# Optimization experiments

Hardware: AMD Instinct MI355X
Metric: run time of the kernel (lower is better)

The kernel has to match this reference:

```python
import jax, jax.numpy as jnp
import numpy as np

BN_EPS = 1e-5

def _vq(x, embed):
    # x: (..., dim), embed: (dim, K). Nearest-codeword lookup with straight-through.
    dim = x.shape[-1]
    flat = x.reshape(-1, dim)
    dist = (flat * flat).sum(1, keepdims=True) - 2.0 * (flat @ embed) + (embed * embed).sum(0, keepdims=True)
    ids = jnp.argmin(dist, axis=1)
    q = jnp.take(embed.T, ids, axis=0).reshape(x.shape)
    diff = jnp.mean((jax.lax.stop_gradient(q) - x) ** 2)
    q = x + jax.lax.stop_gradient(q - x)
    return q, diff

def _weight_quantize(W, embed, in_mem, out_mem):
    # W: (out_f, in_f). Group W.T into (out_g, in_g, in_mem*out_mem) blocks,
    # VQ each block, scatter back to (out_f, in_f). Matches torch chunk/stack loops.
    out_f, in_f = W.shape
    in_g, out_g = in_f // in_mem, out_f // out_mem
    g = W.T.reshape(in_g, in_mem, out_g, out_mem).transpose(2, 0, 1, 3).reshape(out_g, in_g, in_mem * out_mem)
    q, diff = _vq(g, embed)
    qW = q.reshape(out_g, in_g, in_mem, out_mem).transpose(0, 3, 1, 2).reshape(out_f, in_f)
    return qW, diff

def _bn(x, gamma, beta):
    # training-mode BatchNorm1d: biased batch variance
    mu = x.mean(axis=0)
    var = ((x - mu) ** 2).mean(axis=0)
    return (x - mu) * jax.lax.rsqrt(var + BN_EPS) * gamma + beta


def setup_inputs() -> dict:
    key = jax.random.key(0)
    ks = jax.random.split(key, 8)
    B, D_IN, H, D_OUT, K = 65536, 784, 512, 10, 512
    s = 0.05
    return {
        "x": jax.random.normal(ks[0], (B, D_IN), jnp.float32),
        "W1": jax.random.normal(ks[1], (H, D_IN), jnp.float32) * s,
        "b1": jnp.zeros((H,), jnp.float32),
        "gamma1": jnp.ones((H,), jnp.float32),
        "beta1": jnp.zeros((H,), jnp.float32),
        "E1": jax.random.normal(ks[2], (28, K), jnp.float32) * s,  # dim = in_mem(7)*out_mem(4)
        "W2": jax.random.normal(ks[3], (H, H), jnp.float32) * s,
        "b2": jnp.zeros((H,), jnp.float32),
        "E2": jax.random.normal(ks[4], (16, K), jnp.float32) * s,  # dim = in_mem(16)*out_mem(1)
        "W3": jax.random.normal(ks[5], (D_OUT, H), jnp.float32) * s,
        "b3": jnp.zeros((D_OUT,), jnp.float32),
    }


def reference(x, W1, b1, gamma1, beta1, E1, W2, b2, E2, W3, b3):
    qW1, diff1 = _weight_quantize(W1, E1, 7, 4)
    h = jax.nn.relu(x @ qW1.T + b1)
    qW2, diff2 = _weight_quantize(W2, E2, 16, 1)
    h = jax.nn.relu(_bn(h, gamma1, beta1) @ qW2.T + b2)
    out = h @ W3.T + b3
    return out, diff1 + diff2
```

## Files before the change

### kernel.cpp

```cpp
#include <hip/hip_runtime.h>
#include <stdint.h>

#define BATCH   65536
#define D_IN    784
#define KP      800
#define HDIM    512
#define D_OUT   10
#define NCODE   512
#define HT_LD   136

typedef _Float16 f16;
typedef _Float16 f16x8 __attribute__((ext_vector_type(8)));
typedef float    f32x4 __attribute__((ext_vector_type(4)));

__device__ __forceinline__ void gld_lds16(const void* g, void* l) {
  __builtin_amdgcn_global_load_lds((const __attribute__((address_space(1))) void*)g,
                                   (__attribute__((address_space(3))) void*)l, 16, 0, 0);
}

#define MEMFENCE asm volatile("" ::: "memory")
#define BARRIER() do { MEMFENCE; __builtin_amdgcn_s_barrier(); MEMFENCE; } while (0)

__global__ void k_vq1(const float* __restrict__ W1, const float* __restrict__ E1,
                      f16* __restrict__ qW1, float* __restrict__ diffacc) {
  #pragma clang fp contract(off)
  __shared__ float E1s[28 * NCODE];
  __shared__ float Ts[NCODE];
  for (int i = threadIdx.x; i < 28 * NCODE; i += 256) E1s[i] = E1[i];
  __syncthreads();
  for (int k = threadIdx.x; k < NCODE; k += 256) {
    float e0 = E1s[k];
    float t = e0 * e0;
    for (int j = 1; j < 28; ++j) {
      float e = E1s[j * NCODE + k];
      float ee = e * e;
      t = t + ee;
    }
    Ts[k] = t;
  }
  __syncthreads();
  const int wid = threadIdx.x >> 6, lane = threadIdx.x & 63;
  const int bid = blockIdx.x * 4 + wid;
  const int og = bid / 112, ig = bid % 112;
  float v[28], vv[28];
  #pragma unroll
  for (int j = 0; j < 28; ++j) {
    int om = j & 3, im = j >> 2;
    v[j] = W1[(og * 4 + om) * D_IN + ig * 7 + im];
    vv[j] = v[j] * v[j];
  }
  float r[8];
  #pragma unroll
  for (int j = 0; j < 8; ++j) r[j] = vv[j];
  #pragma unroll
  for (int j = 0; j < 8; ++j) r[j] = r[j] + vv[8 + j];
  #pragma unroll
  for (int j = 0; j < 8; ++j) r[j] = r[j] + vv[16 + j];
  float s = ((r[0] + r[1]) + (r[2] + r[3])) + ((r[4] + r[5]) + (r[6] + r[7]));
  s = s + vv[24]; s = s + vv[25]; s = s + vv[26]; s = s + vv[27];

  float bestd = 1e30f; int bestk = 0x7fffffff;
  for (int t = 0; t < 8; ++t) {
    int k = t * 64 + lane;
    float dot = 0.f;
    #pragma unroll
    for (int j = 0; j < 28; ++j) dot = __builtin_fmaf(v[j], E1s[j * NCODE + k], dot);
    float d = (s - 2.0f * dot) + Ts[k];
    if (d < bestd || (d == bestd && k < bestk)) { bestd = d; bestk = k; }
  }
  for (int off = 32; off; off >>= 1) {
    float d2 = __shfl_down(bestd, off, 64);
    int   k2 = __shfl_down(bestk, off, 64);
    if (d2 < bestd || (d2 == bestd && k2 < bestk)) { bestd = d2; bestk = k2; }
  }
  int kstar = __shfl(bestk, 0, 64);
  float sq = 0.f;
  if (lane < 28) {
    int om = lane & 3, im = lane >> 2;
    float q = E1s[lane * NCODE + kstar];
    qW1[(size_t)(og * 4 + om) * KP + ig * 7 + im] = (f16)q;
    float dd = q - v[lane]; sq = dd * dd;
  }
  for (int off = 32; off; off >>= 1) sq += __shfl_down(sq, off, 64);
  if (lane == 0) atomicAdd(&diffacc[bid & 127], sq);
}

__global__ void k_vq2(const float* __restrict__ W2, const float* __restrict__ E2,
                      f16* __restrict__ qW2, float* __restrict__ diffacc) {
  #pragma clang fp contract(off)
  __shared__ float E2s[16 * NCODE];
  __shared__ float Ts[NCODE];
  for (int i = threadIdx.x; i < 16 * NCODE; i += 256) E2s[i] = E2[i];
  __syncthreads();
  for (int k = threadIdx.x; k < NCODE; k += 256) {
    float e0 = E2s[k];
    float t = e0 * e0;
    for (int j = 1; j < 16; ++j) {
      float e = E2s[j * NCODE + k];
      float ee = e * e;
      t = t + ee;
    }
    Ts[k] = t;
  }
  __syncthreads();
  const int wid = threadIdx.x >> 6, lane = threadIdx.x & 63;
  const int bid = blockIdx.x * 4 + wid;
  const int og = bid >> 5, ig = bid & 31;
  float v[16], vv[16];
  #pragma unroll
  for (int j = 0; j < 16; ++j) {
    v[j] = W2[og * HDIM + ig * 16 + j];
    vv[j] = v[j] * v[j];
  }
  float r[8];
  #pragma unroll
  for (int j = 0; j < 8; ++j) r[j] = vv[j];
  #pragma unroll
  for (int j = 0; j < 8; ++j) r[j] = r[j] + vv[8 + j];
  float s = ((r[0] + r[1]) + (r[2] + r[3])) + ((r[4] + r[5]) + (r[6] + r[7]));

  float bestd = 1e30f; int bestk = 0x7fffffff;
  for (int t = 0; t < 8; ++t) {
    int k = t * 64 + lane;
    float dot = 0.f;
    #pragma unroll
    for (int j = 0; j < 16; ++j) dot = __builtin_fmaf(v[j], E2s[j * NCODE + k], dot);
    float d = (s - 2.0f * dot) + Ts[k];
    if (d < bestd || (d == bestd && k < bestk)) { bestd = d; bestk = k; }
  }
  for (int off = 32; off; off >>= 1) {
    float d2 = __shfl_down(bestd, off, 64);
    int   k2 = __shfl_down(bestk, off, 64);
    if (d2 < bestd || (d2 == bestd && k2 < bestk)) { bestd = d2; bestk = k2; }
  }
  int kstar = __shfl(bestk, 0, 64);
  float sq = 0.f;
  if (lane < 16) {
    float q = E2s[lane * NCODE + kstar];
    qW2[(size_t)og * HDIM + ig * 16 + lane] = (f16)q;
    float dd = q - v[lane]; sq = dd * dd;
  }
  for (int off = 32; off; off >>= 1) sq += __shfl_down(sq, off, 64);
  if (lane == 0) atomicAdd(&diffacc[bid & 127], sq);
}

__global__ void __launch_bounds__(256, 4)
k_gemm1(const float* __restrict__ X, const f16* __restrict__ Bw,
        const float* __restrict__ bias, f16* __restrict__ C,
        float* __restrict__ statacc) {
  __shared__ __align__(16) char lds_all[HT_LD * 128 * 2];
  __shared__ float cls[128], cls2[128];
  f16* ht = (f16*)lds_all;
  const int tid = threadIdx.x;
  const int logical = ((blockIdx.x & 7) << 8) + (blockIdx.x >> 3);
  const int bn = logical & 3;
  const int bm = logical >> 2;
  const int lane = tid & 63, wid = tid >> 6;
  const int waveM = wid & 1, waveN = wid >> 1;
  const int l15 = lane & 15, quad = lane >> 4;

  if (tid < 128) cls[tid] = 0.f; else cls2[tid - 128] = 0.f;

  const int cA = tid & 3;
  const int r0 = tid >> 2;
  const float* gX0 = X + (size_t)(bm * 128 + r0) * D_IN;
  const float* gX1 = gX0 + (size_t)64 * D_IN;
  const f16*  gB0 = Bw + (size_t)(bn * 128 + r0) * KP + cA * 8;
  const f16*  gB1 = gB0 + (size_t)64 * KP;

  f32x4 acc[4][4];
  #pragma unroll
  for (int i = 0; i < 4; ++i)
    #pragma unroll
    for (int j = 0; j < 4; ++j) acc[i][j] = (f32x4){0.f, 0.f, 0.f, 0.f};

  const int aoff = (waveM * 64 + l15) * 32 + quad * 8;
  const int boff = (waveN * 64 + l15) * 32 + quad * 8;

  float4 ra0, ra1, ra2, ra3;
  auto issueA = [&](int k0) {
    int gc = k0 + cA * 8;
    int gco = gc < D_IN ? gc : 0;
    ra0 = *(const float4*)(gX0 + gco);
    ra1 = *(const float4*)(gX0 + gco + 4);
    ra2 = *(const float4*)(gX1 + gco);
    ra3 = *(const float4*)(gX1 + gco + 4);
  };
  auto writeA = [&](int k0, f16* dstA) {
    bool valid = (k0 + cA * 8) < D_IN;
    float4 a0 = ra0, a1 = ra1, b0 = ra2, b1 = ra3;
    if (!valid) {
      a0 = (float4){0.f,0.f,0.f,0.f}; a1 = a0; b0 = a0; b1 = a0;
    }
    f16x8 o0, o1;
    o0[0]=(f16)a0.x; o0[1]=(f16)a0.y; o0[2]=(f16)a0.z; o0[3]=(f16)a0.w;
    o0[4]=(f16)a1.x; o0[5]=(f16)a1.y; o0[6]=(f16)a1.z; o0[7]=(f16)a1.w;
    o1[0]=(f16)b0.x; o1[1]=(f16)b0.y; o1[2]=(f16)b0.z; o1[3]=(f16)b0.w;
    o1[4]=(f16)b1.x; o1[5]=(f16)b1.y; o1[6]=(f16)b1.z; o1[7]=(f16)b1.w;
    *(f16x8*)(dstA + tid * 8) = o0;
    *(f16x8*)(dstA + tid * 8 + 2048) = o1;
  };
  auto issueB = [&](int k0, f16* dstB) {
    gld_lds16(gB0 + k0, dstB + tid * 8);
    gld_lds16(gB1 + k0, dstB + tid * 8 + 2048);
  };
  auto mma = [&](const f16* A_, const f16* B_) {
    f16x8 af[4], bf[4];
    #pragma unroll
    for (int i = 0; i < 4; ++i) af[i] = *(const f16x8*)(A_ + aoff + i * 512);
    #pragma unroll
    for (int j = 0; j < 4; ++j) bf[j] = *(const f16x8*)(B_ + boff + j * 512);
    #pragma unroll
    for (int i = 0; i < 4; ++i)
      #pragma unroll
      for (int j = 0; j < 4; ++j)
        acc[i][j] = __builtin_amdgcn_mfma_f32_16x16x32_f16(af[i], bf[j], acc[i][j], 0, 0, 0);
  };

  const int NT = KP / 32;
  issueA(0);
  MEMFENCE;
  issueB(0, (f16*)(lds_all + 16384));
  MEMFENCE;
  writeA(0, (f16*)lds_all);
  issueA(32);
  asm volatile("s_waitcnt vmcnt(4) lgkmcnt(0)" ::: "memory");
  BARRIER();

  for (int k = 0; k < NT; ++k) {
    const int cur = k & 1;
    f16* Asc = (f16*)(lds_all + cur * 8192);
    f16* Bsc = (f16*)(lds_all + 16384 + cur * 8192);
    f16* Asn = (f16*)(lds_all + (cur ^ 1) * 8192);
    f16* Bsn = (f16*)(lds_all + 16384 + (cur ^ 1) * 8192);
    if (k + 1 < NT) issueB((k + 1) * 32, Bsn);
    MEMFENCE;
    __builtin_amdgcn_s_setprio(1);
    mma(Asc, Bsc);
    __builtin_amdgcn_s_setprio(0);
    if (k + 1 < NT) {
      writeA((k + 1) * 32, Asn);
      if (k + 2 < NT) {
        issueA((k + 2) * 32);
        asm volatile("s_waitcnt vmcnt(4) lgkmcnt(0)" ::: "memory");
      } else {
        asm volatile("s_waitcnt vmcnt(0) lgkmcnt(0)" ::: "memory");
      }
    }
    BARRIER();
  }
  const int colbase = bn * 128 + waveN * 64 + l15;
  float bcol[4];
  #pragma unroll
  for (int j = 0; j < 4; ++j) bcol[j] = bias[colbase + j * 16];
  float cs[4] = {0.f,0.f,0.f,0.f}, cs2[4] = {0.f,0.f,0.f,0.f};
  #pragma unroll
  for (int i = 0; i < 4; ++i)
    #pragma unroll
    for (int r2 = 0; r2 < 4; ++r2) {
      int rloc = waveM * 64 + quad * 4 + i * 16 + r2;
      #pragma unroll
      for (int j = 0; j < 4; ++j) {
        float v = acc[i][j][r2] + bcol[j];
        v = v > 0.f ? v : 0.f;
        ht[rloc * HT_LD + waveN * 64 + j * 16 + l15] = (f16)v;
        cs[j] += v; cs2[j] += v * v;
      }
    }
  #pragma unroll
  for (int j = 0; j < 4; ++j) {
    cs[j]  += __shfl_xor(cs[j], 16, 64);  cs[j]  += __shfl_xor(cs[j], 32, 64);
    cs2[j] += __shfl_xor(cs2[j], 16, 64); cs2[j] += __shfl_xor(cs2[j], 32, 64);
  }
  if (quad == 0) {
    #pragma unroll
    for (int j = 0; j < 4; ++j) {
      atomicAdd(&cls[waveN * 64 + j * 16 + l15], cs[j]);
      atomicAdd(&cls2[waveN * 64 + j * 16 + l15], cs2[j]);
    }
  }
  __syncthreads();
  if (tid < 128) atomicAdd(&statacc[256 + bn * 128 + tid], cls[tid]);
  else           atomicAdd(&statacc[768 + bn * 128 + (tid - 128)], cls2[tid - 128]);
  {
    const int rloc = tid >> 1, half = tid & 1;
    f16* crow = C + (size_t)(bm * 128 + rloc) * HDIM + bn * 128 + half * 64;
    const f16* srow = ht + rloc * HT_LD + half * 64;
    #pragma unroll
    for (int j = 0; j < 8; ++j)
      *(f16x8*)(crow + j * 8) = *(const f16x8*)(srow + j * 8);
  }
}

__global__ void k_bnprep(const float* __restrict__ acc, const float* __restrict__ gamma,
                         const float* __restrict__ beta, float* __restrict__ ab,
                         const float* __restrict__ W3, f16* __restrict__ W3h,
                         float* __restrict__ diff_out) {
  const int c = threadIdx.x;
  const float inv = 1.f / 65536.f;
  float mu = acc[256 + c] * inv;
  float msq = acc[768 + c] * inv;
  float var = msq - mu * mu;
  float a = gamma[c] / sqrtf(var + 1e-5f);
  ab[c] = a;
  ab[512 + c] = beta[c] - mu * a;
  #pragma unroll
  for (int o = 0; o < 16; ++o)
    W3h[o * HDIM + c] = (o < D_OUT) ? (f16)W3[o * HDIM + c] : (f16)0.f;
  if (c == 0) {
    float s1 = 0.f, s2 = 0.f;
    for (int i = 0; i < 128; ++i) { s1 += acc[i]; s2 += acc[128 + i]; }
    diff_out[0] = s1 * (1.f / 401408.f) + s2 * (1.f / 262144.f);
  }
}

__global__ void k_bnfold(f16* __restrict__ qW2, const float* __restrict__ ab,
                         const float* __restrict__ b2, float* __restrict__ bias2) {
  __shared__ float red[256];
  const int n = blockIdx.x, t = threadIdx.x;
  float partial = 0.f;
  #pragma unroll
  for (int kk = 0; kk < 2; ++kk) {
    int k = t + kk * 256;
    float w = (float)qW2[n * HDIM + k];
    partial += ab[512 + k] * w;
    qW2[n * HDIM + k] = (f16)(ab[k] * w);
  }
  red[t] = partial; __syncthreads();
  for (int s = 128; s > 0; s >>= 1) { if (t < s) red[t] += red[t + s]; __syncthreads(); }
  if (t == 0) bias2[n] = b2[n] + red[0];
}

__global__ void __launch_bounds__(256, 4)
k_gemm2f(const f16* __restrict__ A, const f16* __restrict__ Bw,
         const float* __restrict__ bias2, const f16* __restrict__ W3h,
         const float* __restrict__ b3, float* __restrict__ out) {
  __shared__ __align__(16) char lds_all[HT_LD * 128 * 2];
  f16* ht = (f16*)lds_all;
  const int tid = threadIdx.x;
  const int logical = ((blockIdx.x & 7) << 8) + (blockIdx.x >> 3);
  const int bn = logical & 3;
  const int bm = logical >> 2;
  const int lane = tid & 63, wid = tid >> 6;
  const int waveM = wid & 1, waveN = wid >> 1;
  const int l15 = lane & 15, quad = lane >> 4;

  const f16* gA0 = A  + (size_t)(bm * 128 + (tid >> 2)) * HDIM + (tid & 3) * 8;
  const f16* gA1 = gA0 + (size_t)64 * HDIM;
  const f16* gB0 = Bw + (size_t)(bn * 128 + (tid >> 2)) * HDIM + (tid & 3) * 8;
  const f16* gB1 = gB0 + (size_t)64 * HDIM;

  f32x4 acc[4][4];
  #pragma unroll
  for (int i = 0; i < 4; ++i)
    #pragma unroll
    for (int j = 0; j < 4; ++j) acc[i][j] = (f32x4){0.f, 0.f, 0.f, 0.f};

  const int aoff = (waveM * 64 + l15) * 32 + quad * 8;
  const int boff = (waveN * 64 + l15) * 32 + quad * 8;

  auto issueT = [&](int k0, int b) {
    f16* As_ = (f16*)(lds_all + b * 8192);
    f16* Bs_ = (f16*)(lds_all + 16384 + b * 8192);
    gld_lds16(gA0 + k0, As_ + tid * 8);
    gld_lds16(gA1 + k0, As_ + tid * 8 + 2048);
    gld_lds16(gB0 + k0, Bs_ + tid * 8);
    gld_lds16(gB1 + k0, Bs_ + tid * 8 + 2048);
  };
  auto mma = [&](const f16* A_, const f16* B_) {
    f16x8 af[4], bf[4];
    #pragma unroll
    for (int i = 0; i < 4; ++i) af[i] = *(const f16x8*)(A_ + aoff + i * 512);
    #pragma unroll
    for (int j = 0; j < 4; ++j) bf[j] = *(const f16x8*)(B_ + boff + j * 512);
    #pragma unroll
    for (int i = 0; i < 4; ++i)
      #pragma unroll
      for (int j = 0; j < 4; ++j)
        acc[i][j] = __builtin_amdgcn_mfma_f32_16x16x32_f16(af[i], bf[j], acc[i][j], 0, 0, 0);
  };

  const int NT = HDIM / 32;
  issueT(0, 0);
  asm volatile("s_waitcnt vmcnt(0)" ::: "memory");
  BARRIER();

  for (int k = 0; k < NT; ++k) {
    const int cur = k & 1;
    if (k + 1 < NT) issueT((k + 1) * 32, cur ^ 1);
    MEMFENCE;
    __builtin_amdgcn_s_setprio(1);
    mma((f16*)(lds_all + cur * 8192), (f16*)(lds_all + 16384 + cur * 8192));
    __builtin_amdgcn_s_setprio(0);
    if (k + 1 < NT) asm volatile("s_waitcnt vmcnt(0)" ::: "memory");
    BARRIER();
  }
  const int colbase = bn * 128 + waveN * 64 + l15;
  float bcol[4];
  #pragma unroll
  for (int j = 0; j < 4; ++j) bcol[j] = bias2[colbase + j * 16];
  #pragma unroll
  for (int i = 0; i < 4; ++i)
    #pragma unroll
    for (int r2 = 0; r2 < 4; ++r2) {
      int rloc = waveM * 64 + quad * 4 + i * 16 + r2;
      #pragma unroll
      for (int j = 0; j < 4; ++j) {
        float v = acc[i][j][r2] + bcol[j];
        v = v > 0.f ? v : 0.f;
        ht[rloc * HT_LD + waveN * 64 + j * 16 + l15] = (f16)v;
      }
    }
  __syncthreads();
  f32x4 oacc[2];
  oacc[0] = (f32x4){0.f,0.f,0.f,0.f}; oacc[1] = (f32x4){0.f,0.f,0.f,0.f};
  #pragma unroll
  for (int ks = 0; ks < 4; ++ks) {
    f16x8 bfr = *(const f16x8*)(W3h + l15 * HDIM + bn * 128 + ks * 32 + quad * 8);
    #pragma unroll
    for (int i2 = 0; i2 < 2; ++i2) {
      f16x8 afr = *(const f16x8*)(ht + (wid * 32 + i2 * 16 + l15) * HT_LD + ks * 32 + quad * 8);
      oacc[i2] = __builtin_amdgcn_mfma_f32_16x16x32_f16(afr, bfr, oacc[i2], 0, 0, 0);
    }
  }
  if (l15 < D_OUT) {
    float badd = (bn == 0) ? b3[l15] : 0.f;
    #pragma unroll
    for (int i2 = 0; i2 < 2; ++i2)
      #pragma unroll
      for (int r2 = 0; r2 < 4; ++r2) {
        int row = bm * 128 + wid * 32 + i2 * 16 + quad * 4 + r2;
        atomicAdd(&out[(size_t)row * D_OUT + l15], oacc[i2][r2] + badd);
      }
  }
}

extern "C" void kernel_launch(void* const* d_in, const int* in_sizes, int n_in,
                              void* d_out, int out_size, void* d_ws, size_t ws_size,
                              hipStream_t stream) {
  const float* x     = (const float*)d_in[0];
  const float* W1    = (const float*)d_in[1];
  const float* b1    = (const float*)d_in[2];
  const float* gamma = (const float*)d_in[3];
  const float* beta  = (const float*)d_in[4];
  const float* E1    = (const float*)d_in[5];
  const float* W2    = (const float*)d_in[6];
  const float* b2    = (const float*)d_in[7];
  const float* E2    = (const float*)d_in[8];
  const float* W3    = (const float*)d_in[9];
  const float* b3    = (const float*)d_in[10];
  float* out = (float*)d_out;

  char* ws = (char*)d_ws;
  float* accum = (float*)ws;
  f16* qW1h = (f16*)(ws + 8192);
  f16* qW2h = (f16*)(ws + 827392);
  f16* W3h  = (f16*)(ws + 1351680);
  float* ab = (float*)(ws + 1368064);
  float* bias2 = (float*)(ws + 1372160);
  f16* h    = (f16*)(ws + 1376256);

  hipMemsetAsync(ws, 0, 827392, stream);
  hipMemsetAsync(d_out, 0, (size_t)out_size * 4, stream);
  k_vq1<<<3584, 256, 0, stream>>>(W1, E1, qW1h, accum);
  k_vq2<<<4096, 256, 0, stream>>>(W2, E2, qW2h, accum + 128);
  k_gemm1<<<2048, 256, 0, stream>>>(x, qW1h, b1, h, accum);
  k_bnprep<<<1, 512, 0, stream>>>(accum, gamma, beta, ab, W3, W3h, out + (size_t)BATCH * D_OUT);
  k_bnfold<<<512, 256, 0, stream>>>(qW2h, ab, b2, bias2);
  k_gemm2f<<<2048, 256, 0, stream>>>(h, qW2h, bias2, W3h, b3, out);
}
```

Measured before the change: 545.9 us.

## Make each GEMM block own a full 128x512 row tile with triple-buffered swizzled LDS

Both GEMM kernels are restructured so that one 512-thread block computes all 512 output columns for its 128 rows, instead of four 256-thread blocks each computing 128 columns. In GEMM1 this removes the fourfold re-read and re-conversion of the fp32 X rows. In the fused second GEMM it lets the final 512-to-10 projection be done entirely inside one block, so outputs are stored directly, with no atomics and no memset of the output. The K loop now uses a three-stage LDS ring that prefetches two steps ahead, with an XOR swizzle on the LDS column chunks to reduce bank conflicts. In exchange it uses far more LDS and registers per block, so occupancy drops to roughly one block per CU and the grid has only 512 blocks.

```diff
diff --git a/kernel.cpp b/kernel.cpp
--- a/kernel.cpp
+++ b/kernel.cpp
@@ -7,7 +7,7 @@
 #define HDIM    512
 #define D_OUT   10
 #define NCODE   512
-#define HT_LD   136
+#define HT_LD   520
 
 typedef _Float16 f16;
 typedef _Float16 f16x8 __attribute__((ext_vector_type(8)));
@@ -144,151 +144,154 @@
   if (lane == 0) atomicAdd(&diffacc[bid & 127], sq);
 }
 
-__global__ void __launch_bounds__(256, 4)
+__global__ void __launch_bounds__(512, 2)
 k_gemm1(const float* __restrict__ X, const f16* __restrict__ Bw,
         const float* __restrict__ bias, f16* __restrict__ C,
         float* __restrict__ statacc) {
   __shared__ __align__(16) char lds_all[HT_LD * 128 * 2];
-  __shared__ float cls[128], cls2[128];
+  __shared__ float cls[512], cls2[512];
   f16* ht = (f16*)lds_all;
   const int tid = threadIdx.x;
-  const int logical = ((blockIdx.x & 7) << 8) + (blockIdx.x >> 3);
-  const int bn = logical & 3;
-  const int bm = logical >> 2;
+  const int bm = blockIdx.x;
   const int lane = tid & 63, wid = tid >> 6;
   const int waveM = wid & 1, waveN = wid >> 1;
   const int l15 = lane & 15, quad = lane >> 4;
 
-  if (tid < 128) cls[tid] = 0.f; else cls2[tid - 128] = 0.f;
-
-  const int cA = tid & 3;
-  const int r0 = tid >> 2;
-  const float* gX0 = X + (size_t)(bm * 128 + r0) * D_IN;
-  const float* gX1 = gX0 + (size_t)64 * D_IN;
-  const f16*  gB0 = Bw + (size_t)(bn * 128 + r0) * KP + cA * 8;
-  const f16*  gB1 = gB0 + (size_t)64 * KP;
-
-  f32x4 acc[4][4];
+  cls[tid] = 0.f; cls2[tid] = 0.f;
+
+  const int rA = tid >> 2, cA = tid & 3;
+  const float* gArow = X + (size_t)(bm * 128 + rA) * D_IN;
+  const int wAoff = rA * 32 + ((cA ^ ((rA >> 1) & 3)) * 8);
+  const f16* gBp[4]; int lBoff[4];
+  #pragma unroll
+  for (int i = 0; i < 4; ++i) {
+    int s = tid + i * 512;
+    int rB = s >> 2, cB = s & 3;
+    gBp[i] = Bw + (size_t)rB * KP + ((cB ^ ((rB >> 1) & 3)) * 8);
+    lBoff[i] = s * 8;
+  }
+
+  f32x4 acc[4][8];
   #pragma unroll
   for (int i = 0; i < 4; ++i)
     #pragma unroll
-    for (int j = 0; j < 4; ++j) acc[i][j] = (f32x4){0.f, 0.f, 0.f, 0.f};
-
-  const int aoff = (waveM * 64 + l15) * 32 + quad * 8;
-  const int boff = (waveN * 64 + l15) * 32 + quad * 8;
-
-  float4 ra0, ra1, ra2, ra3;
+    for (int j = 0; j < 8; ++j) acc[i][j] = (f32x4){0.f, 0.f, 0.f, 0.f};
+
+  const int cs_l = (l15 >> 1) & 3;
+  const int aoff = (waveM * 64 + l15) * 32;
+  const int boff = (waveN * 128 + l15) * 32;
+  const int qoff = (quad ^ cs_l) * 8;
+
+  float4 ra0, ra1;
   auto issueA = [&](int k0) {
     int gc = k0 + cA * 8;
     int gco = gc < D_IN ? gc : 0;
-    ra0 = *(const float4*)(gX0 + gco);
-    ra1 = *(const float4*)(gX0 + gco + 4);
-    ra2 = *(const float4*)(gX1 + gco);
-    ra3 = *(const float4*)(gX1 + gco + 4);
-  };
-  auto writeA = [&](int k0, f16* dstA) {
-    bool valid = (k0 + cA * 8) < D_IN;
-    float4 a0 = ra0, a1 = ra1, b0 = ra2, b1 = ra3;
-    if (!valid) {
-      a0 = (float4){0.f,0.f,0.f,0.f}; a1 = a0; b0 = a0; b1 = a0;
-    }
-    f16x8 o0, o1;
-    o0[0]=(f16)a0.x; o0[1]=(f16)a0.y; o0[2]=(f16)a0.z; o0[3]=(f16)a0.w;
-    o0[4]=(f16)a1.x; o0[5]=(f16)a1.y; o0[6]=(f16)a1.z; o0[7]=(f16)a1.w;
-    o1[0]=(f16)b0.x; o1[1]=(f16)b0.y; o1[2]=(f16)b0.z; o1[3]=(f16)b0.w;
-    o1[4]=(f16)b1.x; o1[5]=(f16)b1.y; o1[6]=(f16)b1.z; o1[7]=(f16)b1.w;
-    *(f16x8*)(dstA + tid * 8) = o0;
-    *(f16x8*)(dstA + tid * 8 + 2048) = o1;
-  };
-  auto issueB = [&](int k0, f16* dstB) {
-    gld_lds16(gB0 + k0, dstB + tid * 8);
-    gld_lds16(gB1 + k0, dstB + tid * 8 + 2048);
-  };
-  auto mma = [&](const f16* A_, const f16* B_) {
-    f16x8 af[4], bf[4];
-    #pragma unroll
-    for (int i = 0; i < 4; ++i) af[i] = *(const f16x8*)(A_ + aoff + i * 512);
-    #pragma unroll
-    for (int j = 0; j < 4; ++j) bf[j] = *(const f16x8*)(B_ + boff + j * 512);
+    ra0 = *(const float4*)(gArow + gco);
+    ra1 = *(const float4*)(gArow + gco + 4);
+  };
+  auto writeA = [&](int k0, char* buf) {
+    float4 a0 = ra0, a1 = ra1;
+    if (k0 + cA * 8 >= D_IN) { a0 = (float4){0.f,0.f,0.f,0.f}; a1 = a0; }
+    f16x8 o;
+    o[0]=(f16)a0.x; o[1]=(f16)a0.y; o[2]=(f16)a0.z; o[3]=(f16)a0.w;
+    o[4]=(f16)a1.x; o[5]=(f16)a1.y; o[6]=(f16)a1.z; o[7]=(f16)a1.w;
+    *(f16x8*)((f16*)buf + wAoff) = o;
+  };
+  auto issueB = [&](int k0, char* buf) {
+    f16* Bs_ = (f16*)(buf + 8192);
+    #pragma unroll
+    for (int i = 0; i < 4; ++i) gld_lds16(gBp[i] + k0, Bs_ + lBoff[i]);
+  };
+  auto mma = [&](const char* buf) {
+    const f16* As_ = (const f16*)buf;
+    const f16* Bs_ = (const f16*)(buf + 8192);
+    f16x8 af[4], bf[8];
+    #pragma unroll
+    for (int i = 0; i < 4; ++i) af[i] = *(const f16x8*)(As_ + aoff + i * 512 + qoff);
+    #pragma unroll
+    for (int j = 0; j < 8; ++j) bf[j] = *(const f16x8*)(Bs_ + boff + j * 512 + qoff);
     #pragma unroll
     for (int i = 0; i < 4; ++i)
       #pragma unroll
-      for (int j = 0; j < 4; ++j)
+      for (int j = 0; j < 8; ++j)
         acc[i][j] = __builtin_amdgcn_mfma_f32_16x16x32_f16(af[i], bf[j], acc[i][j], 0, 0, 0);
   };
 
   const int NT = KP / 32;
-  issueA(0);
+
+  issueA(0);  MEMFENCE;
+  issueB(0, lds_all);          MEMFENCE;
+  issueB(32, lds_all + 40960); MEMFENCE;
+  writeA(0, lds_all);
   MEMFENCE;
-  issueB(0, (f16*)(lds_all + 16384));
-  MEMFENCE;
-  writeA(0, (f16*)lds_all);
-  issueA(32);
-  asm volatile("s_waitcnt vmcnt(4) lgkmcnt(0)" ::: "memory");
+  issueA(32); MEMFENCE;
+  asm volatile("s_waitcnt vmcnt(6) lgkmcnt(0)" ::: "memory");
   BARRIER();
 
+  int cur = 0;
   for (int k = 0; k < NT; ++k) {
-    const int cur = k & 1;
-    f16* Asc = (f16*)(lds_all + cur * 8192);
-    f16* Bsc = (f16*)(lds_all + 16384 + cur * 8192);
-    f16* Asn = (f16*)(lds_all + (cur ^ 1) * 8192);
-    f16* Bsn = (f16*)(lds_all + 16384 + (cur ^ 1) * 8192);
-    if (k + 1 < NT) issueB((k + 1) * 32, Bsn);
+    int n1 = cur + 40960; if (n1 == 122880) n1 = 0;
+    int n2 = n1 + 40960;  if (n2 == 122880) n2 = 0;
+    if (k + 2 < NT) { issueB((k + 2) * 32, lds_all + n2); }
     MEMFENCE;
     __builtin_amdgcn_s_setprio(1);
-    mma(Asc, Bsc);
+    mma(lds_all + cur);
     __builtin_amdgcn_s_setprio(0);
     if (k + 1 < NT) {
-      writeA((k + 1) * 32, Asn);
+      MEMFENCE;
+      writeA((k + 1) * 32, lds_all + n1);
+      MEMFENCE;
       if (k + 2 < NT) {
-        issueA((k + 2) * 32);
-        asm volatile("s_waitcnt vmcnt(4) lgkmcnt(0)" ::: "memory");
+        issueA((k + 2) * 32); MEMFENCE;
+        asm volatile("s_waitcnt vmcnt(6) lgkmcnt(0)" ::: "memory");
       } else {
         asm volatile("s_waitcnt vmcnt(0) lgkmcnt(0)" ::: "memory");
       }
     }
     BARRIER();
-  }
-  const int colbase = bn * 128 + waveN * 64 + l15;
-  float bcol[4];
-  #pragma unroll
-  for (int j = 0; j < 4; ++j) bcol[j] = bias[colbase + j * 16];
-  float cs[4] = {0.f,0.f,0.f,0.f}, cs2[4] = {0.f,0.f,0.f,0.f};
+    cur = n1;
+  }
+
+  const int colbase = waveN * 128 + l15;
+  float bcol[8];
+  #pragma unroll
+  for (int j = 0; j < 8; ++j) bcol[j] = bias[colbase + j * 16];
+  float cs[8], cs2[8];
+  #pragma unroll
+  for (int j = 0; j < 8; ++j) { cs[j] = 0.f; cs2[j] = 0.f; }
   #pragma unroll
   for (int i = 0; i < 4; ++i)
     #pragma unroll
     for (int r2 = 0; r2 < 4; ++r2) {
-      int rloc = waveM * 64 + quad * 4 + i * 16 + r2;
+      int rloc = waveM * 64 + i * 16 + quad * 4 + r2;
       #pragma unroll
-      for (int j = 0; j < 4; ++j) {
+      for (int j = 0; j < 8; ++j) {
         float v = acc[i][j][r2] + bcol[j];
         v = v > 0.f ? v : 0.f;
-        ht[rloc * HT_LD + waveN * 64 + j * 16 + l15] = (f16)v;
+        ht[rloc * HT_LD + waveN * 128 + j * 16 + l15] = (f16)v;
         cs[j] += v; cs2[j] += v * v;
       }
     }
   #pragma unroll
-  for (int j = 0; j < 4; ++j) {
+  for (int j = 0; j < 8; ++j) {
     cs[j]  += __shfl_xor(cs[j], 16, 64);  cs[j]  += __shfl_xor(cs[j], 32, 64);
     cs2[j] += __shfl_xor(cs2[j], 16, 64); cs2[j] += __shfl_xor(cs2[j], 32, 64);
   }
   if (quad == 0) {
     #pragma unroll
-    for (int j = 0; j < 4; ++j) {
-      atomicAdd(&cls[waveN * 64 + j * 16 + l15], cs[j]);
-      atomicAdd(&cls2[waveN * 64 + j * 16 + l15], cs2[j]);
-    }
-  }
-  __syncthreads();
-  if (tid < 128) atomicAdd(&statacc[256 + bn * 128 + tid], cls[tid]);
-  else           atomicAdd(&statacc[768 + bn * 128 + (tid - 128)], cls2[tid - 128]);
-  {
-    const int rloc = tid >> 1, half = tid & 1;
-    f16* crow = C + (size_t)(bm * 128 + rloc) * HDIM + bn * 128 + half * 64;
-    const f16* srow = ht + rloc * HT_LD + half * 64;
-    #pragma unroll
-    for (int j = 0; j < 8; ++j)
-      *(f16x8*)(crow + j * 8) = *(const f16x8*)(srow + j * 8);
+    for (int j = 0; j < 8; ++j) {
+      atomicAdd(&cls[waveN * 128 + j * 16 + l15], cs[j]);
+      atomicAdd(&cls2[waveN * 128 + j * 16 + l15], cs2[j]);
+    }
+  }
+  __syncthreads();
+  atomicAdd(&statacc[256 + tid], cls[tid]);
+  atomicAdd(&statacc[768 + tid], cls2[tid]);
+  #pragma unroll
+  for (int rr = 0; rr < 16; ++rr) {
+    int row = wid * 16 + rr;
+    f16x8 vrow = *(const f16x8*)(ht + row * HT_LD + lane * 8);
+    *(f16x8*)(C + (size_t)(bm * 128 + row) * HDIM + lane * 8) = vrow;
   }
 }
 
@@ -331,107 +334,116 @@
   if (t == 0) bias2[n] = b2[n] + red[0];
 }
 
-__global__ void __launch_bounds__(256, 4)
+__global__ void __launch_bounds__(512, 2)
 k_gemm2f(const f16* __restrict__ A, const f16* __restrict__ Bw,
          const float* __restrict__ bias2, const f16* __restrict__ W3h,
          const float* __restrict__ b3, float* __restrict__ out) {
   __shared__ __align__(16) char lds_all[HT_LD * 128 * 2];
   f16* ht = (f16*)lds_all;
   const int tid = threadIdx.x;
-  const int logical = ((blockIdx.x & 7) << 8) + (blockIdx.x >> 3);
-  const int bn = logical & 3;
-  const int bm = logical >> 2;
+  const int bm = blockIdx.x;
   const int lane = tid & 63, wid = tid >> 6;
   const int waveM = wid & 1, waveN = wid >> 1;
   const int l15 = lane & 15, quad = lane >> 4;
 
-  const f16* gA0 = A  + (size_t)(bm * 128 + (tid >> 2)) * HDIM + (tid & 3) * 8;
-  const f16* gA1 = gA0 + (size_t)64 * HDIM;
-  const f16* gB0 = Bw + (size_t)(bn * 128 + (tid >> 2)) * HDIM + (tid & 3) * 8;
-  const f16* gB1 = gB0 + (size_t)64 * HDIM;
-
-  f32x4 acc[4][4];
+  const int rA = tid >> 2, cA = tid & 3;
+  const f16* gAp = A + (size_t)(bm * 128 + rA) * HDIM + ((cA ^ ((rA >> 1) & 3)) * 8);
+  const int lAoff = tid * 8;
+  const f16* gBp[4]; int lBoff[4];
+  #pragma unroll
+  for (int i = 0; i < 4; ++i) {
+    int s = tid + i * 512;
+    int rB = s >> 2, cB = s & 3;
+    gBp[i] = Bw + (size_t)rB * HDIM + ((cB ^ ((rB >> 1) & 3)) * 8);
+    lBoff[i] = s * 8;
+  }
+
+  f32x4 acc[4][8];
   #pragma unroll
   for (int i = 0; i < 4; ++i)
     #pragma unroll
-    for (int j = 0; j < 4; ++j) acc[i][j] = (f32x4){0.f, 0.f, 0.f, 0.f};
-
-  const int aoff = (waveM * 64 + l15) * 32 + quad * 8;
-  const int boff = (waveN * 64 + l15) * 32 + quad * 8;
-
-  auto issueT = [&](int k0, int b) {
-    f16* As_ = (f16*)(lds_all + b * 8192);
-    f16* Bs_ = (f16*)(lds_all + 16384 + b * 8192);
-    gld_lds16(gA0 + k0, As_ + tid * 8);
-    gld_lds16(gA1 + k0, As_ + tid * 8 + 2048);
-    gld_lds16(gB0 + k0, Bs_ + tid * 8);
-    gld_lds16(gB1 + k0, Bs_ + tid * 8 + 2048);
-  };
-  auto mma = [&](const f16* A_, const f16* B_) {
-    f16x8 af[4], bf[4];
-    #pragma unroll
-    for (int i = 0; i < 4; ++i) af[i] = *(const f16x8*)(A_ + aoff + i * 512);
-    #pragma unroll
-    for (int j = 0; j < 4; ++j) bf[j] = *(const f16x8*)(B_ + boff + j * 512);
+    for (int j = 0; j < 8; ++j) acc[i][j] = (f32x4){0.f, 0.f, 0.f, 0.f};
+
+  const int cs_l = (l15 >> 1) & 3;
+  const int aoff = (waveM * 64 + l15) * 32;
+  const int boff = (waveN * 128 + l15) * 32;
+  const int qoff = (quad ^ cs_l) * 8;
+
+  auto issueT = [&](int k0, char* buf) {
+    f16* As_ = (f16*)buf;
+    f16* Bs_ = (f16*)(buf + 8192);
+    gld_lds16(gAp + k0, As_ + lAoff);
+    #pragma unroll
+    for (int i = 0; i < 4; ++i) gld_lds16(gBp[i] + k0, Bs_ + lBoff[i]);
+  };
+  auto mma = [&](const char* buf) {
+    const f16* As_ = (const f16*)buf;
+    const f16* Bs_ = (const f16*)(buf + 8192);
+    f16x8 af[4], bf[8];
+    #pragma unroll
+    for (int i = 0; i < 4; ++i) af[i] = *(const f16x8*)(As_ + aoff + i * 512 + qoff);
+    #pragma unroll
+    for (int j = 0; j < 8; ++j) bf[j] = *(const f16x8*)(Bs_ + boff + j * 512 + qoff);
     #pragma unroll
     for (int i = 0; i < 4; ++i)
       #pragma unroll
-      for (int j = 0; j < 4; ++j)
+      for (int j = 0; j < 8; ++j)
         acc[i][j] = __builtin_amdgcn_mfma_f32_16x16x32_f16(af[i], bf[j], acc[i][j], 0, 0, 0);
   };
 
   const int NT = HDIM / 32;
-  issueT(0, 0);
-  asm volatile("s_waitcnt vmcnt(0)" ::: "memory");
+
+  issueT(0, lds_all);          MEMFENCE;
+  issueT(32, lds_all + 40960); MEMFENCE;
+  asm volatile("s_waitcnt vmcnt(5)" ::: "memory");
   BARRIER();
 
+  int cur = 0;
   for (int k = 0; k < NT; ++k) {
-    const int cur = k & 1;
-    if (k + 1 < NT) issueT((k + 1) * 32, cur ^ 1);
+    int n1 = cur + 40960; if (n1 == 122880) n1 = 0;
+    int n2 = n1 + 40960;  if (n2 == 122880) n2 = 0;
+    if (k + 2 < NT) { issueT((k + 2) * 32, lds_all + n2); }
     MEMFENCE;
     __builtin_amdgcn_s_setprio(1);
-    mma((f16*)(lds_all + cur * 8192), (f16*)(lds_all + 16384 + cur * 8192));
+    mma(lds_all + cur);
     __builtin_amdgcn_s_setprio(0);
-    if (k + 1 < NT) asm volatile("s_waitcnt vmcnt(0)" ::: "memory");
+    if (k + 2 < NT)      asm volatile("s_waitcnt vmcnt(5)" ::: "memory");
+    else if (k + 1 < NT) asm volatile("s_waitcnt vmcnt(0)" ::: "memory");
     BARRIER();
-  }
-  const int colbase = bn * 128 + waveN * 64 + l15;
-  float bcol[4];
-  #pragma unroll
-  for (int j = 0; j < 4; ++j) bcol[j] = bias2[colbase + j * 16];
+    cur = n1;
+  }
+
+  const int colbase = waveN * 128 + l15;
+  float bcol[8];
+  #pragma unroll
+  for (int j = 0; j < 8; ++j) bcol[j] = bias2[colbase + j * 16];
   #pragma unroll
   for (int i = 0; i < 4; ++i)
     #pragma unroll
     for (int r2 = 0; r2 < 4; ++r2) {
-      int rloc = waveM * 64 + quad * 4 + i * 16 + r2;
+      int rloc = waveM * 64 + i * 16 + quad * 4 + r2;
       #pragma unroll
-      for (int j = 0; j < 4; ++j) {
+      for (int j = 0; j < 8; ++j) {
         float v = acc[i][j][r2] + bcol[j];
         v = v > 0.f ? v : 0.f;
-        ht[rloc * HT_LD + waveN * 64 + j * 16 + l15] = (f16)v;
+        ht[rloc * HT_LD + waveN * 128 + j * 16 + l15] = (f16)v;
       }
     }
   __syncthreads();
-  f32x4 oacc[2];
-  oacc[0] = (f32x4){0.f,0.f,0.f,0.f}; oacc[1] = (f32x4){0.f,0.f,0.f,0.f};
-  #pragma unroll
-  for (int ks = 0; ks < 4; ++ks) {
-    f16x8 bfr = *(const f16x8*)(W3h + l15 * HDIM + bn * 128 + ks * 32 + quad * 8);
-    #pragma unroll
-    for (int i2 = 0; i2 < 2; ++i2) {
-      f16x8 afr = *(const f16x8*)(ht + (wid * 32 + i2 * 16 + l15) * HT_LD + ks * 32 + quad * 8);
-      oacc[i2] = __builtin_amdgcn_mfma_f32_16x16x32_f16(afr, bfr, oacc[i2], 0, 0, 0);
-    }
+  f32x4 oacc = (f32x4){0.f, 0.f, 0.f, 0.f};
+  #pragma unroll
+  for (int ks = 0; ks < 16; ++ks) {
+    f16x8 bfr = *(const f16x8*)(W3h + l15 * HDIM + ks * 32 + quad * 8);
+    f16x8 afr = *(const f16x8*)(ht + (wid * 16 + l15) * HT_LD + ks * 32 + quad * 8);
+    oacc = __builtin_amdgcn_mfma_f32_16x16x32_f16(afr, bfr, oacc, 0, 0, 0);
   }
   if (l15 < D_OUT) {
-    float badd = (bn == 0) ? b3[l15] : 0.f;
-    #pragma unroll
-    for (int i2 = 0; i2 < 2; ++i2)
-      #pragma unroll
-      for (int r2 = 0; r2 < 4; ++r2) {
-        int row = bm * 128 + wid * 32 + i2 * 16 + quad * 4 + r2;
-        atomicAdd(&out[(size_t)row * D_OUT + l15], oacc[i2][r2] + badd);
-      }
+    float badd = b3[l15];
+    #pragma unroll
+    for (int r2 = 0; r2 < 4; ++r2) {
+      int row = bm * 128 + wid * 16 + quad * 4 + r2;
+      out[(size_t)row * D_OUT + l15] = oacc[r2] + badd;
+    }
   }
 }
 
@@ -460,12 +472,11 @@
   float* bias2 = (float*)(ws + 1372160);
   f16* h    = (f16*)(ws + 1376256);
 
-  hipMemsetAsync(ws, 0, 827392, stream);
-  hipMemsetAsync(d_out, 0, (size_t)out_size * 4, stream);
+  (void)hipMemsetAsync(ws, 0, 827392, stream);
   k_vq1<<<3584, 256, 0, stream>>>(W1, E1, qW1h, accum);
   k_vq2<<<4096, 256, 0, stream>>>(W2, E2, qW2h, accum + 128);
-  k_gemm1<<<2048, 256, 0, stream>>>(x, qW1h, b1, h, accum);
+  k_gemm1<<<512, 512, 0, stream>>>(x, qW1h, b1, h, accum);
   k_bnprep<<<1, 512, 0, stream>>>(accum, gamma, beta, ab, W3, W3h, out + (size_t)BATCH * D_OUT);
   k_bnfold<<<512, 256, 0, stream>>>(qW2h, ab, b2, bias2);
-  k_gemm2f<<<2048, 256, 0, stream>>>(h, qW2h, bias2, W3h, b3, out);
-}
+  k_gemm2f<<<512, 512, 0, stream>>>(h, qW2h, bias2, W3h, b3, out);
+}
```

Result: faster. 516.6 us (-5.4%).
